# Performance work log

Measured on AMD Instinct MI355X. Metric: run time of the kernel, lower is better.

Reference implementation:

```python
import jax, jax.numpy as jnp
import numpy as np
import math

B, L = 32, 1000
N_CHAR, EMB, D_MODEL, N_HEADS, PRED_HS, N_OUT = 256, 512, 512, 8, 512, 8
D_HEAD = D_MODEL // N_HEADS


def _pos_encoding(seq_len, d_model, dtype=jnp.float32):
    pos = jnp.arange(seq_len, dtype=dtype)[:, None]                      # [L,1]
    div = jnp.exp(jnp.arange(0, d_model, 2, dtype=dtype) * (-math.log(10000.0) / d_model))
    pe = jnp.zeros((seq_len, d_model), dtype=dtype)
    pe = pe.at[:, 0::2].set(jnp.sin(pos * div))
    pe = pe.at[:, 1::2].set(jnp.cos(pos * div))
    return pe                                                            # [L,D]


def setup_inputs() -> dict:
    key = jax.random.key(0)
    ks = jax.random.split(key, 12)
    def xavier(k, shape):
        fan_in, fan_out = shape[1], shape[0]
        lim = math.sqrt(6.0 / (fan_in + fan_out))
        return jax.random.uniform(k, shape, jnp.float32, -lim, lim)
    data = jax.random.randint(ks[0], (B, L), 0, N_CHAR, dtype=jnp.int64)
    lengths = jnp.clip(jax.random.randint(ks[1], (B,), 0, L, dtype=jnp.int64), 1, L)
    emb = jax.random.normal(ks[2], (N_CHAR, EMB), jnp.float32) * math.sqrt(2.0 / (N_CHAR + EMB))
    return {
        'data': data,
        'lengths': lengths,
        'emb': emb,
        'Wq': xavier(ks[3], (D_MODEL, EMB)), 'bq': jnp.zeros((D_MODEL,), jnp.float32),
        'Wk': xavier(ks[4], (D_MODEL, EMB)), 'bk': jnp.zeros((D_MODEL,), jnp.float32),
        'Wv': xavier(ks[5], (D_MODEL, EMB)), 'bv': jnp.zeros((D_MODEL,), jnp.float32),
        'W1': xavier(ks[6], (PRED_HS, D_MODEL)), 'b1': jnp.full((PRED_HS,), 0.01, jnp.float32),
        'W2': xavier(ks[7], (N_OUT, PRED_HS)), 'b2': jnp.full((N_OUT,), 0.01, jnp.float32),
    }


def reference(data, lengths, emb, Wq, bq, Wk, bk, Wv, bv, W1, b1, W2, b2):
    bs, seq = data.shape
    x = emb[data]                                              # [B,L,E]
    x = x + _pos_encoding(seq, x.shape[-1], x.dtype)[None]     # positional encoding
    # q/k/v projections -> [B,L,H,dh]
    q = (x @ Wq.T + bq).reshape(bs, seq, N_HEADS, D_HEAD)
    k = (x @ Wk.T + bk).reshape(bs, seq, N_HEADS, D_HEAD)
    v = (x @ Wv.T + bv).reshape(bs, seq, N_HEADS, D_HEAD)
    scale = 1.0 / math.sqrt(D_HEAD)
    score = jnp.einsum('bqhd,bkhd->bhqk', q, k) * scale        # [B,H,L,L]
    causal = jnp.tril(jnp.ones((seq, seq), dtype=bool))        # True = keep
    score = jnp.where(causal[None, None], score, -jnp.inf)
    attn = jax.nn.softmax(score, axis=-1)
    ctx = jnp.einsum('bhqk,bkhd->bqhd', attn, v).reshape(bs, seq, D_MODEL)
    # take hidden state at last valid position per sequence
    ctx_last = jnp.take_along_axis(ctx, (lengths - 1)[:, None, None].astype(jnp.int32), axis=1)[:, 0]  # [B,D]
    h = jax.nn.leaky_relu(ctx_last @ W1.T + b1)                # pred layer 1
    out = jax.nn.relu(h @ W2.T + b2)                           # [B,8]
    out = jnp.mean(out, axis=-1)                               # [B]
    return jax.nn.leaky_relu(out)
```

## Files before the change

### kernel.cpp

```cpp
#include <hip/hip_runtime.h>
#include <math.h>

#define BATCH   32
#define LSEQ    1000
#define NHEADS  8
#define DHEAD   64
#define PE_C    (-9.210340371976184f / 512.0f)

__device__ __forceinline__ float pe_val(int j, int e) {
  int ef = e & ~1;
  float dv  = __expf((float)ef * PE_C);
  float arg = (float)j * dv;
  return (e & 1) ? __cosf(arg) : __sinf(arg);
}

__global__ __launch_bounds__(256) void qfold_kernel(
    const int* __restrict__ data, const int* __restrict__ lengths,
    const float* __restrict__ emb,
    const float* __restrict__ Wq, const float* __restrict__ bq,
    const float* __restrict__ Wk, const float* __restrict__ bk,
    float* __restrict__ wfT4, float* __restrict__ bias_dot) {
  int h = blockIdx.x, b = blockIdx.y;
  int p = lengths[b] - 1;
  int t = threadIdx.x;
  __shared__ float xs[512];
  __shared__ float red[256];
  __shared__ float qs[64];
  int tok = data[b * LSEQ + p];
  const float* er = emb + (size_t)tok * 512;
  xs[t]       = er[t]       + pe_val(p, t);
  xs[t + 256] = er[t + 256] + pe_val(p, t + 256);
  __syncthreads();
  int col = h * 64 + (t & 63);
  int kp  = t >> 6;
  {
    const float* wr = Wq + (size_t)col * 512 + kp * 128;
    const float* xp = xs + kp * 128;
    float a = 0.0f;
    for (int e = 0; e < 128; e += 4) {
      float4 wv = *(const float4*)(wr + e);
      a += wv.x * xp[e] + wv.y * xp[e + 1] + wv.z * xp[e + 2] + wv.w * xp[e + 3];
    }
    red[t] = a;
  }
  __syncthreads();
  if (t < 64) {
    float qval = (red[t] + red[t + 64] + red[t + 128] + red[t + 192]
                  + bq[h * 64 + t]) * 0.125f;
    qs[t] = qval;
    float bd = qval * bk[h * 64 + t];
    #pragma unroll
    for (int o = 32; o > 0; o >>= 1) bd += __shfl_xor(bd, o, 64);
    if (t == 0) bias_dot[b * NHEADS + h] = bd;
  }
  __syncthreads();
  float a0 = 0.0f, a1 = 0.0f;
  const float* wkb = Wk + (size_t)(h * 64) * 512;
  for (int d = 0; d < 64; ++d) {
    float qd = qs[d];
    a0 += qd * wkb[d * 512 + t];
    a1 += qd * wkb[d * 512 + t + 256];
  }
  int bh = b * NHEADS + h;
  int e1 = t, e2 = t + 256;
  wfT4[(e1 >> 2) * 1024 + bh * 4 + (e1 & 3)] = a0;
  wfT4[(e2 >> 2) * 1024 + bh * 4 + (e2 & 3)] = a1;
}

__global__ __launch_bounds__(256) void foldmd_kernel(
    const float* __restrict__ emb, const float* __restrict__ wfT4,
    const float* __restrict__ bias_dot, float* __restrict__ MD) {
  __shared__ float rows[8 * 512];
  int t   = threadIdx.x;
  int r0  = blockIdx.x * 8;
  int bh0 = blockIdx.y * 64;
  #pragma unroll
  for (int i = 0; i < 4; ++i) {
    int fi = t + i * 256;
    int rr = fi >> 7;
    int e  = (fi & 127) * 4;
    int rg = r0 + rr;
    float4 v;
    if (rg < 256) {
      v = *(const float4*)(emb + (size_t)rg * 512 + e);
    } else {
      int j = rg - 256;
      float dv0 = __expf((float)e * PE_C);
      float dv1 = __expf((float)(e + 2) * PE_C);
      float a0 = (float)j * dv0, a1 = (float)j * dv1;
      v.x = __sinf(a0); v.y = __cosf(a0);
      v.z = __sinf(a1); v.w = __cosf(a1);
    }
    *(float4*)(&rows[rr * 512 + e]) = v;
  }
  __syncthreads();
  int bh_l = t & 63;
  int rp   = t >> 6;
  const float* rw0 = rows + (2 * rp) * 512;
  const float* rw1 = rows + (2 * rp + 1) * 512;
  const float* wp  = wfT4 + (bh0 + bh_l) * 4;
  float a0 = 0.0f, a1 = 0.0f;
  #pragma unroll 8
  for (int g = 0; g < 128; ++g) {
    float4 w4 = *(const float4*)(wp + g * 1024);
    float4 v0 = *(const float4*)(rw0 + 4 * g);
    float4 v1 = *(const float4*)(rw1 + 4 * g);
    a0 += v0.x * w4.x + v0.y * w4.y + v0.z * w4.z + v0.w * w4.w;
    a1 += v1.x * w4.x + v1.y * w4.y + v1.z * w4.z + v1.w * w4.w;
  }
  float bd = (r0 < 256) ? bias_dot[bh0 + bh_l] : 0.0f;
  MD[(size_t)(r0 + 2 * rp)     * 256 + bh0 + bh_l] = a0 + bd;
  MD[(size_t)(r0 + 2 * rp + 1) * 256 + bh0 + bh_l] = a1 + bd;
}

__global__ __launch_bounds__(256) void attn_ypass_kernel(
    const int* __restrict__ data, const int* __restrict__ lengths,
    const float* __restrict__ emb, const float* __restrict__ MD,
    float* __restrict__ mS, float* __restrict__ y_part) {
  int jc = blockIdx.x, b = blockIdx.y;
  int n = lengths[b];
  int j0 = jc * 125;
  if (j0 >= n) return;
  int cnt = min(125, n - j0);
  int t = threadIdx.x;
  __shared__ float sl[125][8];
  __shared__ int   tk[125];
  __shared__ float redw[4][8];
  __shared__ float m_sh[8], s_sh[8];
  const float* Edot = MD;
  const float* Pdot = MD + 256 * 256;
  if (t < 125) {
    if (t < cnt) {
      int tok = data[b * LSEQ + j0 + t];
      tk[t] = tok;
      const float* er = Edot + (size_t)tok * 256 + b * 8;
      const float* pr = Pdot + (size_t)(j0 + t) * 256 + b * 8;
      float4 e0 = *(const float4*)(er);
      float4 e1 = *(const float4*)(er + 4);
      float4 p0 = *(const float4*)(pr);
      float4 p1 = *(const float4*)(pr + 4);
      sl[t][0] = e0.x + p0.x; sl[t][1] = e0.y + p0.y;
      sl[t][2] = e0.z + p0.z; sl[t][3] = e0.w + p0.w;
      sl[t][4] = e1.x + p1.x; sl[t][5] = e1.y + p1.y;
      sl[t][6] = e1.z + p1.z; sl[t][7] = e1.w + p1.w;
    } else {
      #pragma unroll
      for (int h = 0; h < 8; ++h) sl[t][h] = -INFINITY;
    }
  }
  __syncthreads();
  int h = t & 7, jg = t >> 3, w = t >> 6;
  {
    float m = -INFINITY;
    for (int j = jg; j < 125; j += 32) m = fmaxf(m, sl[j][h]);
    #pragma unroll
    for (int o = 8; o < 64; o <<= 1) m = fmaxf(m, __shfl_xor(m, o, 64));
    if ((t & 63) < 8) redw[w][t & 7] = m;
  }
  __syncthreads();
  if (t < 8)
    m_sh[t] = fmaxf(fmaxf(redw[0][t], redw[1][t]),
                    fmaxf(redw[2][t], redw[3][t]));
  __syncthreads();
  {
    float mh = m_sh[h];
    float sum = 0.0f;
    for (int j = jg; j < 125; j += 32) {
      float p = __expf(sl[j][h] - mh);
      sl[j][h] = p;
      sum += p;
    }
    #pragma unroll
    for (int o = 8; o < 64; o <<= 1) sum += __shfl_xor(sum, o, 64);
    if ((t & 63) < 8) redw[w][t & 7] = sum;
  }
  __syncthreads();
  if (t < 8)
    s_sh[t] = redw[0][t] + redw[1][t] + redw[2][t] + redw[3][t];
  __syncthreads();
  int lane = t & 63;
  int e0i = w * 128 + lane * 2;
  float dv = __expf((float)e0i * PE_C);
  float acc0[8] = {0,0,0,0,0,0,0,0};
  float acc1[8] = {0,0,0,0,0,0,0,0};
  for (int jj = 0; jj < cnt; ++jj) {
    int tok = tk[jj];
    float2 ev = *(const float2*)(emb + (size_t)tok * 512 + e0i);
    float arg = (float)(j0 + jj) * dv;
    float x0 = ev.x + __sinf(arg);
    float x1 = ev.y + __cosf(arg);
    #pragma unroll
    for (int hh = 0; hh < 8; ++hh) {
      float pj = sl[jj][hh];
      acc0[hh] += pj * x0;
      acc1[hh] += pj * x1;
    }
  }
  size_t base = (size_t)(b * 8 + jc) * 4096 + e0i;
  #pragma unroll
  for (int hh = 0; hh < 8; ++hh) {
    float2 o; o.x = acc0[hh]; o.y = acc1[hh];
    *(float2*)(y_part + base + hh * 512) = o;
  }
  if (t < 8) {
    float2 ms; ms.x = m_sh[t]; ms.y = s_sh[t];
    *(float2*)(mS + ((size_t)(b * 8 + jc) * 8 + t) * 2) = ms;
  }
}

__global__ __launch_bounds__(256) void ctx_kernel(
    const int* __restrict__ lengths, const float* __restrict__ y_part,
    const float* __restrict__ mS, const float* __restrict__ Wv,
    const float* __restrict__ bv, float* __restrict__ ctx) {
  int h = blockIdx.x, b = blockIdx.y;
  int t = threadIdx.x;
  __shared__ float ys[512];
  __shared__ float red[256];
  int n = lengths[b];
  int nc = (n + 124) / 125;
  float M = -INFINITY;
  for (int jc = 0; jc < nc; ++jc)
    M = fmaxf(M, mS[((size_t)(b * 8 + jc) * 8 + h) * 2]);
  float S = 0.0f, s0 = 0.0f, s1 = 0.0f;
  for (int jc = 0; jc < nc; ++jc) {
    float2 ms = *(const float2*)(mS + ((size_t)(b * 8 + jc) * 8 + h) * 2);
    float wgt = __expf(ms.x - M);
    S += wgt * ms.y;
    size_t base = (size_t)(b * 8 + jc) * 4096 + h * 512;
    s0 += wgt * y_part[base + t];
    s1 += wgt * y_part[base + t + 256];
  }
  float inv = 1.0f / S;
  ys[t]       = s0 * inv;
  ys[t + 256] = s1 * inv;
  __syncthreads();
  int col = h * 64 + (t & 63);
  int kp  = t >> 6;
  const float* wr = Wv + (size_t)col * 512 + kp * 128;
  const float* xp = ys + kp * 128;
  float a = 0.0f;
  for (int e = 0; e < 128; e += 4) {
    float4 wv4 = *(const float4*)(wr + e);
    a += wv4.x * xp[e] + wv4.y * xp[e + 1] + wv4.z * xp[e + 2] + wv4.w * xp[e + 3];
  }
  red[t] = a;
  __syncthreads();
  if (t < 64)
    ctx[b * 512 + h * 64 + t] =
        red[t] + red[t + 64] + red[t + 128] + red[t + 192] + bv[h * 64 + t];
}

__global__ __launch_bounds__(256) void mlp1_kernel(
    const float* __restrict__ ctx, const float* __restrict__ W1,
    const float* __restrict__ b1, float* __restrict__ hs) {
  int chunk = blockIdx.x, b = blockIdx.y;
  int t = threadIdx.x;
  __shared__ float xs[512];
  __shared__ float red[256];
  xs[t]       = ctx[b * 512 + t];
  xs[t + 256] = ctx[b * 512 + t + 256];
  __syncthreads();
  int col = chunk * 64 + (t & 63);
  int kp  = t >> 6;
  const float* wr = W1 + (size_t)col * 512 + kp * 128;
  const float* xp = xs + kp * 128;
  float a = 0.0f;
  for (int e = 0; e < 128; e += 4) {
    float4 wv = *(const float4*)(wr + e);
    a += wv.x * xp[e] + wv.y * xp[e + 1] + wv.z * xp[e + 2] + wv.w * xp[e + 3];
  }
  red[t] = a;
  __syncthreads();
  if (t < 64) {
    float v = red[t] + red[t + 64] + red[t + 128] + red[t + 192] + b1[chunk * 64 + t];
    hs[b * 512 + chunk * 64 + t] = (v > 0.0f) ? v : 0.01f * v;
  }
}

__global__ __launch_bounds__(256) void mlp2_kernel(
    const float* __restrict__ hs, const float* __restrict__ W2,
    const float* __restrict__ b2, float* __restrict__ out) {
  int b = blockIdx.x, t = threadIdx.x;
  __shared__ float o8[8];
  int j = t >> 5, sub = t & 31;
  const float* hr  = hs + (size_t)b * 512;
  const float* w2r = W2 + (size_t)j * 512;
  float part = 0.0f;
  for (int e = sub * 16; e < sub * 16 + 16; e += 4) {
    float4 wv = *(const float4*)(w2r + e);
    float4 hv = *(const float4*)(hr + e);
    part += wv.x * hv.x + wv.y * hv.y + wv.z * hv.z + wv.w * hv.w;
  }
  #pragma unroll
  for (int o = 16; o > 0; o >>= 1) part += __shfl_xor(part, o, 64);
  if (sub == 0) o8[j] = fmaxf(part + b2[j], 0.0f);
  __syncthreads();
  if (t == 0) {
    float m = 0.0f;
    #pragma unroll
    for (int i = 0; i < 8; ++i) m += o8[i];
    m *= 0.125f;
    out[b] = (m > 0.0f) ? m : 0.01f * m;
  }
}

extern "C" void kernel_launch(void* const* d_in, const int* in_sizes, int n_in,
                              void* d_out, int out_size, void* d_ws, size_t ws_size,
                              hipStream_t stream) {
  const int*   data    = (const int*)d_in[0];
  const int*   lengths = (const int*)d_in[1];
  const float* emb     = (const float*)d_in[2];
  const float* Wq      = (const float*)d_in[3];
  const float* bq      = (const float*)d_in[4];
  const float* Wk      = (const float*)d_in[5];
  const float* bk      = (const float*)d_in[6];
  const float* Wv      = (const float*)d_in[7];
  const float* bv      = (const float*)d_in[8];
  const float* W1      = (const float*)d_in[9];
  const float* b1      = (const float*)d_in[10];
  const float* W2      = (const float*)d_in[11];
  const float* b2      = (const float*)d_in[12];
  float* out = (float*)d_out;

  char* ws = (char*)d_ws;
  float* wfT4     = (float*)(ws);
  float* MD       = (float*)(ws + 524288);
  float* bias_dot = (float*)(ws + 1810432);
  float* mS       = (float*)(ws + 1811456);
  float* y_part   = (float*)(ws + 1827840);
  float* ctx      = (float*)(ws + 6022144);
  float* hs       = (float*)(ws + 6087680);

  dim3 g1(NHEADS, BATCH);
  qfold_kernel<<<g1, 256, 0, stream>>>(data, lengths, emb, Wq, bq, Wk, bk,
                                       wfT4, bias_dot);
  dim3 g2(157, 4);
  foldmd_kernel<<<g2, 256, 0, stream>>>(emb, wfT4, bias_dot, MD);
  dim3 g3(8, BATCH);
  attn_ypass_kernel<<<g3, 256, 0, stream>>>(data, lengths, emb, MD, mS, y_part);
  dim3 g4(NHEADS, BATCH);
  ctx_kernel<<<g4, 256, 0, stream>>>(lengths, y_part, mS, Wv, bv, ctx);
  dim3 g5(8, BATCH);
  mlp1_kernel<<<g5, 256, 0, stream>>>(ctx, W1, b1, hs);
  mlp2_kernel<<<BATCH, 256, 0, stream>>>(hs, W2, b2, out);
}
```

Before: 140.2 us.

## Shrink attention chunks, precompute PE table, and pad shared rows

Cuts the per-block key chunk from 125 to 64 and doubles the number of chunk blocks per batch, giving more parallel blocks for the sequential y-pass loop. The positional-encoding table is written once by foldmd and read in the y-pass instead of recomputing sin/cos for each element. Score computation now uses registers with two keys per thread instead of shared-memory passes. The foldmd shared rows are padded to avoid bank conflicts. In exchange, y_part and mS roughly double in size, which adds merge work in ctx_kernel, and the PE table adds a global read stream.

```diff
diff --git a/kernel.cpp b/kernel.cpp
--- a/kernel.cpp
+++ b/kernel.cpp
@@ -5,6 +5,8 @@
 #define LSEQ    1000
 #define NHEADS  8
 #define DHEAD   64
+#define CHUNK   64
+#define NCHUNK  16
 #define PE_C    (-9.210340371976184f / 512.0f)
 
 __device__ __forceinline__ float pe_val(int j, int e) {
@@ -69,8 +71,9 @@
 
 __global__ __launch_bounds__(256) void foldmd_kernel(
     const float* __restrict__ emb, const float* __restrict__ wfT4,
-    const float* __restrict__ bias_dot, float* __restrict__ MD) {
-  __shared__ float rows[8 * 512];
+    const float* __restrict__ bias_dot, float* __restrict__ MD,
+    float* __restrict__ pe_tab) {
+  __shared__ float rows[8 * 516];
   int t   = threadIdx.x;
   int r0  = blockIdx.x * 8;
   int bh0 = blockIdx.y * 64;
@@ -90,113 +93,108 @@
       float a0 = (float)j * dv0, a1 = (float)j * dv1;
       v.x = __sinf(a0); v.y = __cosf(a0);
       v.z = __sinf(a1); v.w = __cosf(a1);
+      if (blockIdx.y == 0)
+        *(float4*)(pe_tab + (size_t)j * 512 + e) = v;
     }
-    *(float4*)(&rows[rr * 512 + e]) = v;
-  }
-  __syncthreads();
-  int bh_l = t & 63;
-  int rp   = t >> 6;
-  const float* rw0 = rows + (2 * rp) * 512;
-  const float* rw1 = rows + (2 * rp + 1) * 512;
-  const float* wp  = wfT4 + (bh0 + bh_l) * 4;
+    *(float4*)(&rows[rr * 516 + e]) = v;
+  }
+  __syncthreads();
+  int w    = t >> 6, lane = t & 63;
+  int bh   = bh0 + w * 16 + (lane & 15);
+  int rp   = lane >> 4;
+  const float* rw0 = rows + (2 * rp) * 516;
+  const float* rw1 = rows + (2 * rp + 1) * 516;
+  const float* wp  = wfT4 + (size_t)bh * 4;
   float a0 = 0.0f, a1 = 0.0f;
   #pragma unroll 8
   for (int g = 0; g < 128; ++g) {
-    float4 w4 = *(const float4*)(wp + g * 1024);
+    float4 w4 = *(const float4*)(wp + (size_t)g * 1024);
     float4 v0 = *(const float4*)(rw0 + 4 * g);
     float4 v1 = *(const float4*)(rw1 + 4 * g);
     a0 += v0.x * w4.x + v0.y * w4.y + v0.z * w4.z + v0.w * w4.w;
     a1 += v1.x * w4.x + v1.y * w4.y + v1.z * w4.z + v1.w * w4.w;
   }
-  float bd = (r0 < 256) ? bias_dot[bh0 + bh_l] : 0.0f;
-  MD[(size_t)(r0 + 2 * rp)     * 256 + bh0 + bh_l] = a0 + bd;
-  MD[(size_t)(r0 + 2 * rp + 1) * 256 + bh0 + bh_l] = a1 + bd;
+  float bd = (r0 < 256) ? bias_dot[bh] : 0.0f;
+  int r = r0 + 2 * rp;
+  MD[(size_t)r * 256 + bh]       = a0 + bd;
+  MD[(size_t)(r + 1) * 256 + bh] = a1 + bd;
 }
 
 __global__ __launch_bounds__(256) void attn_ypass_kernel(
     const int* __restrict__ data, const int* __restrict__ lengths,
     const float* __restrict__ emb, const float* __restrict__ MD,
+    const float* __restrict__ pe_tab,
     float* __restrict__ mS, float* __restrict__ y_part) {
   int jc = blockIdx.x, b = blockIdx.y;
   int n = lengths[b];
-  int j0 = jc * 125;
+  int j0 = jc * CHUNK;
   if (j0 >= n) return;
-  int cnt = min(125, n - j0);
+  int cnt = min(CHUNK, n - j0);
   int t = threadIdx.x;
-  __shared__ float sl[125][8];
-  __shared__ int   tk[125];
+  __shared__ float sl[CHUNK][8];
+  __shared__ int   tk[CHUNK];
   __shared__ float redw[4][8];
   __shared__ float m_sh[8], s_sh[8];
   const float* Edot = MD;
   const float* Pdot = MD + 256 * 256;
-  if (t < 125) {
-    if (t < cnt) {
-      int tok = data[b * LSEQ + j0 + t];
-      tk[t] = tok;
-      const float* er = Edot + (size_t)tok * 256 + b * 8;
-      const float* pr = Pdot + (size_t)(j0 + t) * 256 + b * 8;
-      float4 e0 = *(const float4*)(er);
-      float4 e1 = *(const float4*)(er + 4);
-      float4 p0 = *(const float4*)(pr);
-      float4 p1 = *(const float4*)(pr + 4);
-      sl[t][0] = e0.x + p0.x; sl[t][1] = e0.y + p0.y;
-      sl[t][2] = e0.z + p0.z; sl[t][3] = e0.w + p0.w;
-      sl[t][4] = e1.x + p1.x; sl[t][5] = e1.y + p1.y;
-      sl[t][6] = e1.z + p1.z; sl[t][7] = e1.w + p1.w;
-    } else {
-      #pragma unroll
-      for (int h = 0; h < 8; ++h) sl[t][h] = -INFINITY;
-    }
-  }
-  __syncthreads();
-  int h = t & 7, jg = t >> 3, w = t >> 6;
-  {
-    float m = -INFINITY;
-    for (int j = jg; j < 125; j += 32) m = fmaxf(m, sl[j][h]);
-    #pragma unroll
-    for (int o = 8; o < 64; o <<= 1) m = fmaxf(m, __shfl_xor(m, o, 64));
-    if ((t & 63) < 8) redw[w][t & 7] = m;
-  }
+
+  if (t < CHUNK) tk[t] = data[b * LSEQ + j0 + ((t < cnt) ? t : 0)];
+  __syncthreads();
+
+  int h = t & 7, jA = t >> 3, jB = jA + 32;
+  int bh8 = b * 8 + h;
+  float sA = -INFINITY, sB = -INFINITY;
+  if (jA < cnt)
+    sA = Edot[(size_t)tk[jA] * 256 + bh8] + Pdot[(size_t)(j0 + jA) * 256 + bh8];
+  if (jB < cnt)
+    sB = Edot[(size_t)tk[jB] * 256 + bh8] + Pdot[(size_t)(j0 + jB) * 256 + bh8];
+
+  int w = t >> 6;
+  float mloc = fmaxf(sA, sB);
+  #pragma unroll
+  for (int o = 8; o < 64; o <<= 1) mloc = fmaxf(mloc, __shfl_xor(mloc, o, 64));
+  if ((t & 63) < 8) redw[w][t & 7] = mloc;
   __syncthreads();
   if (t < 8)
     m_sh[t] = fmaxf(fmaxf(redw[0][t], redw[1][t]),
                     fmaxf(redw[2][t], redw[3][t]));
   __syncthreads();
-  {
-    float mh = m_sh[h];
-    float sum = 0.0f;
-    for (int j = jg; j < 125; j += 32) {
-      float p = __expf(sl[j][h] - mh);
-      sl[j][h] = p;
-      sum += p;
-    }
-    #pragma unroll
-    for (int o = 8; o < 64; o <<= 1) sum += __shfl_xor(sum, o, 64);
-    if ((t & 63) < 8) redw[w][t & 7] = sum;
-  }
-  __syncthreads();
-  if (t < 8)
-    s_sh[t] = redw[0][t] + redw[1][t] + redw[2][t] + redw[3][t];
-  __syncthreads();
+  float mh = m_sh[h];
+  float pA = __expf(sA - mh);
+  float pB = __expf(sB - mh);
+  sl[jA][h] = pA;
+  sl[jB][h] = pB;
+  float sloc = pA + pB;
+  #pragma unroll
+  for (int o = 8; o < 64; o <<= 1) sloc += __shfl_xor(sloc, o, 64);
+  if ((t & 63) < 8) redw[w][t & 7] = sloc;
+  __syncthreads();
+  if (t < 8) s_sh[t] = redw[0][t] + redw[1][t] + redw[2][t] + redw[3][t];
+
   int lane = t & 63;
   int e0i = w * 128 + lane * 2;
-  float dv = __expf((float)e0i * PE_C);
-  float acc0[8] = {0,0,0,0,0,0,0,0};
-  float acc1[8] = {0,0,0,0,0,0,0,0};
+  float acc0[8] = {0, 0, 0, 0, 0, 0, 0, 0};
+  float acc1[8] = {0, 0, 0, 0, 0, 0, 0, 0};
+  const float* pe_row = pe_tab + (size_t)j0 * 512 + e0i;
+  #pragma unroll 4
   for (int jj = 0; jj < cnt; ++jj) {
     int tok = tk[jj];
     float2 ev = *(const float2*)(emb + (size_t)tok * 512 + e0i);
-    float arg = (float)(j0 + jj) * dv;
-    float x0 = ev.x + __sinf(arg);
-    float x1 = ev.y + __cosf(arg);
-    #pragma unroll
-    for (int hh = 0; hh < 8; ++hh) {
-      float pj = sl[jj][hh];
-      acc0[hh] += pj * x0;
-      acc1[hh] += pj * x1;
-    }
-  }
-  size_t base = (size_t)(b * 8 + jc) * 4096 + e0i;
+    float2 pv = *(const float2*)(pe_row + (size_t)jj * 512);
+    float x0 = ev.x + pv.x;
+    float x1 = ev.y + pv.y;
+    float4 pa = *(const float4*)(&sl[jj][0]);
+    float4 pb = *(const float4*)(&sl[jj][4]);
+    acc0[0] += pa.x * x0; acc1[0] += pa.x * x1;
+    acc0[1] += pa.y * x0; acc1[1] += pa.y * x1;
+    acc0[2] += pa.z * x0; acc1[2] += pa.z * x1;
+    acc0[3] += pa.w * x0; acc1[3] += pa.w * x1;
+    acc0[4] += pb.x * x0; acc1[4] += pb.x * x1;
+    acc0[5] += pb.y * x0; acc1[5] += pb.y * x1;
+    acc0[6] += pb.z * x0; acc1[6] += pb.z * x1;
+    acc0[7] += pb.w * x0; acc1[7] += pb.w * x1;
+  }
+  size_t base = (size_t)(b * NCHUNK + jc) * 4096 + e0i;
   #pragma unroll
   for (int hh = 0; hh < 8; ++hh) {
     float2 o; o.x = acc0[hh]; o.y = acc1[hh];
@@ -204,7 +202,7 @@
   }
   if (t < 8) {
     float2 ms; ms.x = m_sh[t]; ms.y = s_sh[t];
-    *(float2*)(mS + ((size_t)(b * 8 + jc) * 8 + t) * 2) = ms;
+    *(float2*)(mS + ((size_t)(b * NCHUNK + jc) * 8 + t) * 2) = ms;
   }
 }
 
@@ -217,16 +215,16 @@
   __shared__ float ys[512];
   __shared__ float red[256];
   int n = lengths[b];
-  int nc = (n + 124) / 125;
+  int nc = (n + CHUNK - 1) / CHUNK;
   float M = -INFINITY;
   for (int jc = 0; jc < nc; ++jc)
-    M = fmaxf(M, mS[((size_t)(b * 8 + jc) * 8 + h) * 2]);
+    M = fmaxf(M, mS[((size_t)(b * NCHUNK + jc) * 8 + h) * 2]);
   float S = 0.0f, s0 = 0.0f, s1 = 0.0f;
   for (int jc = 0; jc < nc; ++jc) {
-    float2 ms = *(const float2*)(mS + ((size_t)(b * 8 + jc) * 8 + h) * 2);
+    float2 ms = *(const float2*)(mS + ((size_t)(b * NCHUNK + jc) * 8 + h) * 2);
     float wgt = __expf(ms.x - M);
     S += wgt * ms.y;
-    size_t base = (size_t)(b * 8 + jc) * 4096 + h * 512;
+    size_t base = (size_t)(b * NCHUNK + jc) * 4096 + h * 512;
     s0 += wgt * y_part[base + t];
     s1 += wgt * y_part[base + t + 256];
   }
@@ -327,17 +325,19 @@
   float* MD       = (float*)(ws + 524288);
   float* bias_dot = (float*)(ws + 1810432);
   float* mS       = (float*)(ws + 1811456);
-  float* y_part   = (float*)(ws + 1827840);
-  float* ctx      = (float*)(ws + 6022144);
-  float* hs       = (float*)(ws + 6087680);
+  float* y_part   = (float*)(ws + 1844224);
+  float* ctx      = (float*)(ws + 10232832);
+  float* hs       = (float*)(ws + 10298368);
+  float* pe_tab   = (float*)(ws + 10363904);
 
   dim3 g1(NHEADS, BATCH);
   qfold_kernel<<<g1, 256, 0, stream>>>(data, lengths, emb, Wq, bq, Wk, bk,
                                        wfT4, bias_dot);
   dim3 g2(157, 4);
-  foldmd_kernel<<<g2, 256, 0, stream>>>(emb, wfT4, bias_dot, MD);
-  dim3 g3(8, BATCH);
-  attn_ypass_kernel<<<g3, 256, 0, stream>>>(data, lengths, emb, MD, mS, y_part);
+  foldmd_kernel<<<g2, 256, 0, stream>>>(emb, wfT4, bias_dot, MD, pe_tab);
+  dim3 g3(NCHUNK, BATCH);
+  attn_ypass_kernel<<<g3, 256, 0, stream>>>(data, lengths, emb, MD, pe_tab,
+                                            mS, y_part);
   dim3 g4(NHEADS, BATCH);
   ctx_kernel<<<g4, 256, 0, stream>>>(lengths, y_part, mS, Wv, bv, ctx);
   dim3 g5(8, BATCH);
```

Result: slower. 144.9 us (+3.3%).
